# Kernel optimization log

Hardware: AMD Instinct MI355X
Metric: run time of the kernel (lower is better)

The kernel has to match this reference:

```python
import jax, jax.numpy as jnp
import numpy as np

N_CELLS = 50000
N_GENES = 2000
HIDDEN = 128
HEADS = 4
HEAD_DIM = HIDDEN // HEADS
E_FULL = 800000
E_PRUNED = 400000
LN_EPS = 1e-6
NEG_SLOPE = 0.2


def setup_inputs() -> dict:
    key = jax.random.key(0)
    ks = jax.random.split(key, 20)
    s_in = 1.0 / np.sqrt(N_GENES)
    s_h = 1.0 / np.sqrt(HIDDEN)
    inp = {
        "node_features": jax.random.normal(ks[0], (N_CELLS, N_GENES), jnp.float32),
        "full_edge_index": jax.random.randint(ks[1], (2, E_FULL), 0, N_CELLS, jnp.int64 if jax.config.jax_enable_x64 else jnp.int32),
        "full_edge_weights": jax.random.uniform(ks[2], (E_FULL, 1), jnp.float32),
        "pruned_edge_index": jax.random.randint(ks[3], (2, E_PRUNED), 0, N_CELLS, jnp.int64 if jax.config.jax_enable_x64 else jnp.int32),
        "pruned_edge_weights": jax.random.uniform(ks[4], (E_PRUNED, 1), jnp.float32),
        "alpha": jax.random.uniform(ks[5], (), jnp.float32),
        # input projection
        "ip_w": jax.random.normal(ks[6], (N_GENES, HIDDEN), jnp.float32) * s_in,
        "ip_b": jnp.zeros((HIDDEN,), jnp.float32),
        # GAT full graph
        "gf_wsrc": jax.random.normal(ks[7], (HIDDEN, HIDDEN), jnp.float32) * s_h,
        "gf_wdst": jax.random.normal(ks[8], (HIDDEN, HIDDEN), jnp.float32) * s_h,
        "gf_wedge": jax.random.normal(ks[9], (1, HIDDEN), jnp.float32),
        "gf_attn": jax.random.normal(ks[10], (HEADS, HEAD_DIM), jnp.float32) * (1.0 / np.sqrt(HEAD_DIM)),
        "gf_bias": jnp.zeros((HIDDEN,), jnp.float32),
        # GAT pruned graph
        "gp_wsrc": jax.random.normal(ks[11], (HIDDEN, HIDDEN), jnp.float32) * s_h,
        "gp_wdst": jax.random.normal(ks[12], (HIDDEN, HIDDEN), jnp.float32) * s_h,
        "gp_wedge": jax.random.normal(ks[13], (1, HIDDEN), jnp.float32),
        "gp_attn": jax.random.normal(ks[14], (HEADS, HEAD_DIM), jnp.float32) * (1.0 / np.sqrt(HEAD_DIM)),
        "gp_bias": jnp.zeros((HIDDEN,), jnp.float32),
        # LayerNorm
        "ln_scale": jnp.ones((HIDDEN,), jnp.float32),
        "ln_bias": jnp.zeros((HIDDEN,), jnp.float32),
    }
    return inp


def _gatv2(h, edge_index, edge_w, wsrc, wdst, wedge, attn, bias):
    """GATv2 with edge features: e_ij = a_h . leaky_relu(Ws h_i + Wd h_j + We w_ij),
    segment-softmax over destination nodes, scatter-aggregate Ws h_src, concat heads."""
    n = h.shape[0]
    src, dst = edge_index[0], edge_index[1]
    hs = (h @ wsrc).reshape(n, HEADS, HEAD_DIM)
    hd = (h @ wdst).reshape(n, HEADS, HEAD_DIM)
    ew = (edge_w @ wedge).reshape(-1, HEADS, HEAD_DIM)  # [E,H,D]
    z = jax.nn.leaky_relu(hs[src] + hd[dst] + ew, NEG_SLOPE)  # [E,H,D]
    logits = jnp.einsum('ehd,hd->eh', z, attn)  # [E,H]
    # segment softmax over incoming edges of each dst node
    m = jax.ops.segment_max(logits, dst, num_segments=n)
    m = jnp.where(jnp.isfinite(m), m, 0.0)
    ex = jnp.exp(logits - m[dst])
    denom = jax.ops.segment_sum(ex, dst, num_segments=n)
    att = ex / (denom[dst] + 1e-16)  # [E,H]
    out = jax.ops.segment_sum(att[..., None] * hs[src], dst, num_segments=n)  # [n,H,D]
    return out.reshape(n, HIDDEN) + bias


def _layer_norm(x, scale, bias):
    mu = jnp.mean(x, axis=-1, keepdims=True)
    var = jnp.mean(jnp.square(x - mu), axis=-1, keepdims=True)
    return (x - mu) * jax.lax.rsqrt(var + LN_EPS) * scale + bias


def reference(node_features, full_edge_index, full_edge_weights, pruned_edge_index,
              pruned_edge_weights, alpha, ip_w, ip_b,
              gf_wsrc, gf_wdst, gf_wedge, gf_attn, gf_bias,
              gp_wsrc, gp_wdst, gp_wedge, gp_attn, gp_bias,
              ln_scale, ln_bias):
    h = node_features @ ip_w + ip_b  # [n, hidden]
    h_full = _gatv2(h, full_edge_index, full_edge_weights, gf_wsrc, gf_wdst, gf_wedge, gf_attn, gf_bias)
    h_pruned = _gatv2(h, pruned_edge_index, pruned_edge_weights, gp_wsrc, gp_wdst, gp_wedge, gp_attn, gp_bias)
    h = (1.0 - alpha) * h_full + alpha * h_pruned
    h = jax.nn.elu(h)
    return _layer_norm(h, ln_scale, ln_bias)
```

## Files before the change

kernel.cpp:

```cpp
#include <hip/hip_runtime.h>
#include <hip/hip_bf16.h>

#define N_GENES 2000
#define SA 72
#define SH 136

typedef __attribute__((ext_vector_type(8))) short frag8;
typedef __attribute__((ext_vector_type(4))) float facc4;

static __device__ __forceinline__ unsigned short f2bf(float f) {
    unsigned int u = __float_as_uint(f);
    unsigned int r = (u + 0x7FFFu + ((u >> 16) & 1u)) >> 16;
    return (unsigned short)r;
}
static __device__ __forceinline__ float bf2f(unsigned short s) {
    return __uint_as_float(((unsigned int)s) << 16);
}
static __device__ __forceinline__ ushort2 pk2(float a, float b) {
    __hip_bfloat162 r = __float22bfloat162_rn(float2{a, b});
    return *(ushort2*)&r;
}

__global__ void prep(const float* __restrict__ ip_w,
                     const float* __restrict__ ws_f, const float* __restrict__ wd_f,
                     const float* __restrict__ ws_p, const float* __restrict__ wd_p,
                     unsigned short* __restrict__ Bt1,
                     unsigned short* __restrict__ Bf, unsigned short* __restrict__ Bp,
                     int* __restrict__ deg, int n2) {
    int idx = blockIdx.x * blockDim.x + threadIdx.x;
    if (idx < n2) deg[idx] = 0;
    if (idx < 128 * 2048) {
        int nrow = idx >> 11, k = idx & 2047;
        unsigned short v = 0;
        if (k < N_GENES) v = f2bf(ip_w[(size_t)k * 128 + nrow]);
        Bt1[idx] = v;
    } else {
        int q = idx - 128 * 2048;
        if (q >= 2 * 256 * 128) return;
        int g = q >> 15;
        int r = (q >> 7) & 255;
        int k = q & 127;
        const float* w = (g == 0) ? (r < 128 ? ws_f : wd_f) : (r < 128 ? ws_p : wd_p);
        (g == 0 ? Bf : Bp)[(r << 7) | k] = f2bf(w[k * 128 + (r & 127)]);
    }
}

__global__ __launch_bounds__(256) void gemm_deg(const float* __restrict__ A,
                                                const unsigned short* __restrict__ Bt,
                                                const float* __restrict__ bias,
                                                const unsigned short* __restrict__ Bf,
                                                const unsigned short* __restrict__ Bp,
                                                unsigned short* __restrict__ Cf,
                                                unsigned short* __restrict__ Cp,
                                                int M, int K, int gemmBlocks,
                                                const int* __restrict__ dst_f, int Ef,
                                                const int* __restrict__ dst_p, int Ep,
                                                int* __restrict__ deg, int N) {
    if (blockIdx.x >= gemmBlocks) {
        int e = (blockIdx.x - gemmBlocks) * 256 + threadIdx.x;
        if (e < Ef) atomicAdd(&deg[dst_f[e]], 1);
        else if (e < Ef + Ep) atomicAdd(&deg[N + dst_p[e - Ef]], 1);
        return;
    }
    const int Kpad = 2048;
    __shared__ __align__(16) unsigned short lA[64 * SA];
    __shared__ __align__(16) unsigned short lH[64 * SH];
    int t = threadIdx.x, lane = t & 63, wv = t >> 6;
    int lr = lane & 15, lq = lane >> 4;
    facc4 acc[4][2];
#pragma unroll
    for (int i = 0; i < 4; i++)
#pragma unroll
        for (int j = 0; j < 2; j++) acc[i][j] = (facc4){0.f, 0.f, 0.f, 0.f};
    int row_base = blockIdx.x * 64;

    int ar_r[4], ar_c[4];
    const float* ar_p[4];
#pragma unroll
    for (int j = 0; j < 4; j++) {
        int q = j * 256 + t;
        ar_r[j] = q >> 4;
        ar_c[j] = (q & 15) * 4;
        int rg = row_base + ar_r[j];
        if (rg >= M) rg = M - 1;
        ar_p[j] = A + (size_t)rg * K + ar_c[j];
    }
    const unsigned short* bp[4];
#pragma unroll
    for (int ks = 0; ks < 2; ks++)
#pragma unroll
        for (int ni = 0; ni < 2; ni++) {
            int col = wv * 32 + ni * 16 + lr;
            bp[ks * 2 + ni] = Bt + (size_t)col * Kpad + ks * 32 + lq * 8;
        }

    float4 ar[4];
    frag8 bfr[4];
#pragma unroll
    for (int j = 0; j < 4; j++) ar[j] = *(const float4*)(ar_p[j]);
#pragma unroll
    for (int f = 0; f < 4; f++) bfr[f] = *(const frag8*)(bp[f]);

    for (int k0 = 0; k0 < Kpad; k0 += 64) {
        __syncthreads();
#pragma unroll
        for (int j = 0; j < 4; j++) {
            ushort2 u01 = pk2(ar[j].x, ar[j].y);
            ushort2 u23 = pk2(ar[j].z, ar[j].w);
            ushort4 u = {u01.x, u01.y, u23.x, u23.y};
            *(ushort4*)&lA[ar_r[j] * SA + ar_c[j]] = u;
        }
        __syncthreads();
        int kn = k0 + 64;
        frag8 bfn[4];
        if (kn < Kpad) {
#pragma unroll
            for (int j = 0; j < 4; j++) {
                int kk = kn + ar_c[j];
                float4 v = {0.f, 0.f, 0.f, 0.f};
                if (kk < K) v = *(const float4*)(ar_p[j] + kn);
                ar[j] = v;
            }
#pragma unroll
            for (int f = 0; f < 4; f++) bfn[f] = *(const frag8*)(bp[f] + kn);
        }
#pragma unroll
        for (int ks = 0; ks < 2; ks++) {
            frag8 af[4];
#pragma unroll
            for (int mi = 0; mi < 4; mi++)
                af[mi] = *(const frag8*)&lA[(mi * 16 + lr) * SA + ks * 32 + lq * 8];
#pragma unroll
            for (int mi = 0; mi < 4; mi++)
#pragma unroll
                for (int ni = 0; ni < 2; ni++)
                    acc[mi][ni] = __builtin_amdgcn_mfma_f32_16x16x32_bf16(af[mi], bfr[ks * 2 + ni], acc[mi][ni], 0, 0, 0);
        }
        if (kn < Kpad) {
#pragma unroll
            for (int f = 0; f < 4; f++) bfr[f] = bfn[f];
        }
    }
    __syncthreads();
#pragma unroll
    for (int mi = 0; mi < 4; mi++) {
#pragma unroll
        for (int r = 0; r < 4; r++) {
            int row = mi * 16 + lq * 4 + r;
#pragma unroll
            for (int ni = 0; ni < 2; ni++) {
                int col = wv * 32 + ni * 16 + lr;
                lH[row * SH + col] = f2bf(acc[mi][ni][r] + bias[col]);
            }
        }
    }
    __syncthreads();
#pragma unroll 1
    for (int g = 0; g < 2; g++) {
        const unsigned short* B2 = g ? Bp : Bf;
        unsigned short* Cb = g ? Cp : Cf;
        facc4 a2[4][4];
#pragma unroll
        for (int i = 0; i < 4; i++)
#pragma unroll
            for (int j = 0; j < 4; j++) a2[i][j] = (facc4){0.f, 0.f, 0.f, 0.f};
#pragma unroll
        for (int ks = 0; ks < 4; ks++) {
            frag8 af[4], bf[4];
#pragma unroll
            for (int mi = 0; mi < 4; mi++)
                af[mi] = *(const frag8*)&lH[(mi * 16 + lr) * SH + ks * 32 + lq * 8];
#pragma unroll
            for (int ni = 0; ni < 4; ni++)
                bf[ni] = *(const frag8*)(B2 + ((wv * 64 + ni * 16 + lr) << 7) + ks * 32 + lq * 8);
#pragma unroll
            for (int mi = 0; mi < 4; mi++)
#pragma unroll
                for (int ni = 0; ni < 4; ni++)
                    a2[mi][ni] = __builtin_amdgcn_mfma_f32_16x16x32_bf16(af[mi], bf[ni], a2[mi][ni], 0, 0, 0);
        }
#pragma unroll
        for (int mi = 0; mi < 4; mi++) {
#pragma unroll
            for (int r = 0; r < 4; r++) {
                int row = row_base + mi * 16 + lq * 4 + r;
                if (row < M) {
#pragma unroll
                    for (int ni = 0; ni < 4; ni++) {
                        int col = wv * 64 + ni * 16 + lr;
                        Cb[(size_t)row * 256 + col] = f2bf(a2[mi][ni][r]);
                    }
                }
            }
        }
    }
}

__global__ __launch_bounds__(256) void scan_part(const int* __restrict__ in,
                                                 int* __restrict__ bsum, int n) {
    int t = threadIdx.x, b = blockIdx.x;
    int lane = t & 63, wv = t >> 6;
    int base = b * 2048 + t * 8;
    int s = 0;
    if (base + 7 < n) {
        int4 v0 = *(const int4*)(in + base);
        int4 v1 = *(const int4*)(in + base + 4);
        s = v0.x + v0.y + v0.z + v0.w + v1.x + v1.y + v1.z + v1.w;
    } else {
#pragma unroll
        for (int j = 0; j < 8; j++) if (base + j < n) s += in[base + j];
    }
#pragma unroll
    for (int o = 32; o >= 1; o >>= 1) s += __shfl_xor(s, o);
    __shared__ int red[4];
    if (lane == 0) red[wv] = s;
    __syncthreads();
    if (t == 0) bsum[b] = red[0] + red[1] + red[2] + red[3];
}

__global__ __launch_bounds__(256) void scan_tops(int* __restrict__ bsum, int nb,
                                                 int* __restrict__ offs, int n) {
    __shared__ int buf[256];
    int t = threadIdx.x;
    int orig = (t < nb) ? bsum[t] : 0;
    int v = orig;
    buf[t] = v;
    __syncthreads();
    for (int o = 1; o < 256; o <<= 1) {
        int y = (t >= o) ? buf[t - o] : 0;
        __syncthreads();
        v += y;
        buf[t] = v;
        __syncthreads();
    }
    if (t < nb) bsum[t] = v - orig;
    if (t == nb - 1) offs[n] = v;
}

__global__ __launch_bounds__(256) void scan_final(const int* __restrict__ in,
                                                  const int* __restrict__ bsum,
                                                  int* __restrict__ offs, int n) {
    int t = threadIdx.x, b = blockIdx.x;
    int lane = t & 63, wv = t >> 6;
    int base = b * 2048 + t * 8;
    int a[8];
#pragma unroll
    for (int j = 0; j < 8; j++) a[j] = (base + j < n) ? in[base + j] : 0;
    int s = a[0] + a[1] + a[2] + a[3] + a[4] + a[5] + a[6] + a[7];
    int incl = s;
#pragma unroll
    for (int o = 1; o < 64; o <<= 1) {
        int y = __shfl_up(incl, o);
        if (lane >= o) incl += y;
    }
    __shared__ int wsum[4];
    if (lane == 63) wsum[wv] = incl;
    __syncthreads();
    int wpre = 0;
#pragma unroll
    for (int j = 0; j < 4; j++) if (j < wv) wpre += wsum[j];
    int excl = incl - s + wpre + bsum[b];
#pragma unroll
    for (int j = 0; j < 8; j++) {
        if (base + j < n) offs[base + j] = excl;
        excl += a[j];
    }
}

__global__ void fill2(const int* __restrict__ src_f, const int* __restrict__ dst_f,
                      const float* __restrict__ ew_f, int Ef,
                      const int* __restrict__ src_p, const int* __restrict__ dst_p,
                      const float* __restrict__ ew_p, int Ep,
                      const int* __restrict__ offs, int* __restrict__ deg,
                      int2* __restrict__ srcw, int N) {
    int e = blockIdx.x * blockDim.x + threadIdx.x;
    if (e >= Ef + Ep) return;
    int g = (e >= Ef);
    int ee = g ? e - Ef : e;
    int d = g ? dst_p[ee] : dst_f[ee];
    int node = g ? N + d : d;
    int p = offs[node] + atomicAdd(&deg[node], -1) - 1;
    int s = g ? src_p[ee] : src_f[ee];
    float w = g ? ew_p[ee] : ew_f[ee];
    srcw[p] = make_int2(s, __float_as_int(w));
}

__global__ __launch_bounds__(256) void gat2(const int* __restrict__ offs,
                                            const int2* __restrict__ srcw,
                                            const unsigned short* __restrict__ hshd_f,
                                            const unsigned short* __restrict__ hshd_p,
                                            const float* __restrict__ wedge_f,
                                            const float* __restrict__ attn_f,
                                            const float* __restrict__ bias_f,
                                            const float* __restrict__ wedge_p,
                                            const float* __restrict__ attn_p,
                                            const float* __restrict__ bias_p,
                                            float* __restrict__ out_full,
                                            float* __restrict__ out_pruned, int N) {
    int node = blockIdx.x * 4 + (threadIdx.x >> 6);
    if (node >= 2 * N) return;
    int g = node >= N;
    int onode = g ? node - N : node;
    const unsigned short* hshd = g ? hshd_p : hshd_f;
    const float* wedge = g ? wedge_p : wedge_f;
    const float* attn = g ? attn_p : attn_f;
    const float* bias = g ? bias_p : bias_f;
    float* out = g ? out_pruned : out_full;
    int lane = threadIdx.x & 63;
    int d2 = lane * 2;
    const float LOG2E = 1.4426950408889634f;
    const float2 wv = *(const float2*)&wedge[d2];
    float2 av = *(const float2*)&attn[d2];
    av.x *= LOG2E; av.y *= LOG2E;
    unsigned int hdraw = *(const unsigned int*)&hshd[(size_t)onode * 256 + 128 + d2];
    const float hd0 = __uint_as_float(hdraw << 16);
    const float hd1 = __uint_as_float(hdraw & 0xffff0000u);
    int s = offs[node], cnt = offs[node + 1] - s;
    float m = -INFINITY, l = 0.f, acc0 = 0.f, acc1 = 0.f;
    if (cnt > 0) {
        int last = s + cnt - 1;
        auto CL = [last](int j) { return j > last ? last : j; };
        int2 e0 = srcw[s], e1 = srcw[CL(s + 1)], e2 = srcw[CL(s + 2)], e3 = srcw[CL(s + 3)];
        int2 e4 = srcw[CL(s + 4)], e5 = srcw[CL(s + 5)];
        unsigned int hr0 = *(const unsigned int*)&hshd[(size_t)e0.x * 256 + d2];
        unsigned int hr1 = *(const unsigned int*)&hshd[(size_t)e1.x * 256 + d2];
        unsigned int hr2 = *(const unsigned int*)&hshd[(size_t)e2.x * 256 + d2];
        unsigned int hr3 = *(const unsigned int*)&hshd[(size_t)e3.x * 256 + d2];
        for (int i = 0; i < cnt; i += 2) {
            int2 ea = srcw[CL(s + i + 6)], eb = srcw[CL(s + i + 7)];
            unsigned int hr4 = *(const unsigned int*)&hshd[(size_t)e4.x * 256 + d2];
            unsigned int hr5 = *(const unsigned int*)&hshd[(size_t)e5.x * 256 + d2];
            {
                float h0 = __uint_as_float(hr0 << 16);
                float h1 = __uint_as_float(hr0 & 0xffff0000u);
                float w = __int_as_float(e0.y);
                float z0 = fmaf(w, wv.x, h0 + hd0); z0 = (z0 > 0.f) ? z0 : 0.2f * z0;
                float z1 = fmaf(w, wv.y, h1 + hd1); z1 = (z1 > 0.f) ? z1 : 0.2f * z1;
                float t = z0 * av.x + z1 * av.y;
                t += __shfl_xor(t, 1);
                t += __shfl_xor(t, 2);
                t += __shfl_xor(t, 4);
                t += __shfl_xor(t, 8);
                float mn = fmaxf(m, t);
                float sc = __builtin_amdgcn_exp2f(m - mn);
                float p = __builtin_amdgcn_exp2f(t - mn);
                l = l * sc + p;
                acc0 = acc0 * sc + p * h0;
                acc1 = acc1 * sc + p * h1;
                m = mn;
            }
            if (i + 1 < cnt) {
                float h0 = __uint_as_float(hr1 << 16);
                float h1 = __uint_as_float(hr1 & 0xffff0000u);
                float w = __int_as_float(e1.y);
                float z0 = fmaf(w, wv.x, h0 + hd0); z0 = (z0 > 0.f) ? z0 : 0.2f * z0;
                float z1 = fmaf(w, wv.y, h1 + hd1); z1 = (z1 > 0.f) ? z1 : 0.2f * z1;
                float t = z0 * av.x + z1 * av.y;
                t += __shfl_xor(t, 1);
                t += __shfl_xor(t, 2);
                t += __shfl_xor(t, 4);
                t += __shfl_xor(t, 8);
                float mn = fmaxf(m, t);
                float sc = __builtin_amdgcn_exp2f(m - mn);
                float p = __builtin_amdgcn_exp2f(t - mn);
                l = l * sc + p;
                acc0 = acc0 * sc + p * h1 * 0.f + p * h0;
                acc0 = acc0 - p * h0 + p * h0;
                acc0 = acc0;
                acc1 = acc1 * sc + p * h1;
                m = mn;
            }
            e0 = e2; e1 = e3; e2 = e4; e3 = e5; e4 = ea; e5 = eb;
            hr0 = hr2; hr1 = hr3; hr2 = hr4; hr3 = hr5;
        }
    }
    float inv = 1.f / (l + 1e-16f);
    const float2 bv = *(const float2*)&bias[d2];
    float2 o;
    o.x = acc0 * inv + bv.x;
    o.y = acc1 * inv + bv.y;
    *(float2*)&out[(size_t)onode * 128 + d2] = o;
}

__global__ __launch_bounds__(256) void final_kernel(const float* __restrict__ hf,
                                                    float* __restrict__ out,
                                                    const float* __restrict__ alpha_p,
                                                    const float* __restrict__ scale,
                                                    const float* __restrict__ beta, int n) {
    int node = blockIdx.x * 4 + (threadIdx.x >> 6);
    if (node >= n) return;
    int lane = threadIdx.x & 63;
    int d2 = lane * 2;
    float a = *alpha_p;
    float2 f = *(const float2*)&hf[(size_t)node * 128 + d2];
    float2 p = *(const float2*)&out[(size_t)node * 128 + d2];
    float x0 = (1.f - a) * f.x + a * p.x;
    float x1 = (1.f - a) * f.y + a * p.y;
    x0 = (x0 > 0.f) ? x0 : expm1f(x0);
    x1 = (x1 > 0.f) ? x1 : expm1f(x1);
    float sm = x0 + x1;
#pragma unroll
    for (int o = 32; o >= 1; o >>= 1) sm += __shfl_xor(sm, o);
    float mu = sm * (1.f / 128.f);
    float d0 = x0 - mu, d1 = x1 - mu;
    float v = d0 * d0 + d1 * d1;
#pragma unroll
    for (int o = 32; o >= 1; o >>= 1) v += __shfl_xor(v, o);
    float rstd = rsqrtf(v * (1.f / 128.f) + 1e-6f);
    const float2 sv = *(const float2*)&scale[d2];
    const float2 bv = *(const float2*)&beta[d2];
    float2 o2;
    o2.x = d0 * rstd * sv.x + bv.x;
    o2.y = d1 * rstd * sv.y + bv.y;
    *(float2*)&out[(size_t)node * 128 + d2] = o2;
}

extern "C" void kernel_launch(void* const* d_in, const int* in_sizes, int n_in,
                              void* d_out, int out_size, void* d_ws, size_t ws_size,
                              hipStream_t stream) {
    const float* nf = (const float*)d_in[0];
    const int* fei = (const int*)d_in[1];
    const float* few = (const float*)d_in[2];
    const int* pei = (const int*)d_in[3];
    const float* pew = (const float*)d_in[4];
    const float* alpha = (const float*)d_in[5];
    const float* ip_w = (const float*)d_in[6];
    const float* ip_b = (const float*)d_in[7];
    const float* gf_wsrc = (const float*)d_in[8];
    const float* gf_wdst = (const float*)d_in[9];
    const float* gf_wedge = (const float*)d_in[10];
    const float* gf_attn = (const float*)d_in[11];
    const float* gf_bias = (const float*)d_in[12];
    const float* gp_wsrc = (const float*)d_in[13];
    const float* gp_wdst = (const float*)d_in[14];
    const float* gp_wedge = (const float*)d_in[15];
    const float* gp_attn = (const float*)d_in[16];
    const float* gp_bias = (const float*)d_in[17];
    const float* ln_scale = (const float*)d_in[18];
    const float* ln_bias = (const float*)d_in[19];

    const int N = in_sizes[0] / N_GENES;
    const int Ef = in_sizes[1] / 2;
    const int Ep = in_sizes[3] / 2;
    const int Etot = Ef + Ep;
    const int n2 = 2 * N;

    char* base = (char*)d_ws;
    size_t off = 0;
    auto carve = [&](size_t bytes) -> char* {
        char* p = base + off;
        off = (off + bytes + 255) & ~(size_t)255;
        return p;
    };
    unsigned short* Bt1 = (unsigned short*)carve((size_t)128 * 2048 * 2);
    unsigned short* Bf = (unsigned short*)carve(256 * 128 * 2);
    unsigned short* Bp = (unsigned short*)carve(256 * 128 * 2);
    unsigned short* hshd_f = (unsigned short*)carve((size_t)N * 256 * 2);
    unsigned short* hshd_p = (unsigned short*)carve((size_t)N * 256 * 2);
    float* h_full = (float*)carve((size_t)N * 128 * 4);
    int* deg = (int*)carve((size_t)n2 * 4);
    int* offs = (int*)carve((size_t)(n2 + 4) * 4);
    int* bsum = (int*)carve(256 * 4);
    int2* srcw = (int2*)carve((size_t)Etot * 8);
    float* out_f = (float*)d_out;

    const int* src_f = fei;
    const int* dst_f = fei + Ef;
    const int* src_p = pei;
    const int* dst_p = pei + Ep;

    prep<<<(128 * 2048 + 2 * 256 * 128 + 255) / 256, 256, 0, stream>>>(
        ip_w, gf_wsrc, gf_wdst, gp_wsrc, gp_wdst, Bt1, Bf, Bp, deg, n2);

    int gb1 = (N + 63) / 64;
    int degb = (Etot + 255) / 256;
    gemm_deg<<<gb1 + degb, 256, 0, stream>>>(nf, Bt1, ip_b, Bf, Bp, hshd_f, hshd_p,
                                             N, N_GENES, gb1,
                                             dst_f, Ef, dst_p, Ep, deg, N);

    int nb = (n2 + 2047) / 2048;
    scan_part<<<nb, 256, 0, stream>>>(deg, bsum, n2);
    scan_tops<<<1, 256, 0, stream>>>(bsum, nb, offs, n2);
    scan_final<<<nb, 256, 0, stream>>>(deg, bsum, offs, n2);
    fill2<<<(Etot + 255) / 256, 256, 0, stream>>>(src_f, dst_f, few, Ef, src_p, dst_p, pew, Ep,
                                                  offs, deg, srcw, N);

    gat2<<<(n2 + 3) / 4, 256, 0, stream>>>(offs, srcw, hshd_f, hshd_p,
                                           gf_wedge, gf_attn, gf_bias,
                                           gp_wedge, gp_attn, gp_bias,
                                           h_full, out_f, N);

    final_kernel<<<(N + 3) / 4, 256, 0, stream>>>(h_full, out_f, alpha, ln_scale, ln_bias, N);
    (void)ws_size; (void)n_in; (void)out_size;
}
```

Measured before the change: 813.1 us.

## Replace three-pass scan with atomic segment assignment and fuse GAT with final LayerNorm

The three-kernel exclusive scan is replaced by one kernel. Each wavefront scans its degrees and claims a base offset through a global atomic counter, so segments are contiguous but no longer in node order. The fill step now uses a separate cursor array, and degrees are kept for the segment lengths. The two GAT passes and the final blend/ELU/LayerNorm kernel are fused into one kernel per node, removing the h_full round-trip and two launches. Fusion halves the grid to N blocks, each doing both graphs serially, which may lengthen the critical path per wave.

```diff
diff --git a/kernel.cpp b/kernel.cpp
--- a/kernel.cpp
+++ b/kernel.cpp
@@ -12,9 +12,6 @@
     unsigned int u = __float_as_uint(f);
     unsigned int r = (u + 0x7FFFu + ((u >> 16) & 1u)) >> 16;
     return (unsigned short)r;
-}
-static __device__ __forceinline__ float bf2f(unsigned short s) {
-    return __uint_as_float(((unsigned int)s) << 16);
 }
 static __device__ __forceinline__ ushort2 pk2(float a, float b) {
     __hip_bfloat162 r = __float22bfloat162_rn(float2{a, b});
@@ -26,9 +23,10 @@
                      const float* __restrict__ ws_p, const float* __restrict__ wd_p,
                      unsigned short* __restrict__ Bt1,
                      unsigned short* __restrict__ Bf, unsigned short* __restrict__ Bp,
-                     int* __restrict__ deg, int n2) {
+                     int* __restrict__ deg, unsigned int* __restrict__ counter, int n2) {
     int idx = blockIdx.x * blockDim.x + threadIdx.x;
     if (idx < n2) deg[idx] = 0;
+    if (idx == 0) counter[0] = 0u;
     if (idx < 128 * 2048) {
         int nrow = idx >> 11, k = idx & 2047;
         unsigned short v = 0;
@@ -196,118 +194,50 @@
     }
 }
 
-__global__ __launch_bounds__(256) void scan_part(const int* __restrict__ in,
-                                                 int* __restrict__ bsum, int n) {
-    int t = threadIdx.x, b = blockIdx.x;
-    int lane = t & 63, wv = t >> 6;
-    int base = b * 2048 + t * 8;
-    int s = 0;
-    if (base + 7 < n) {
-        int4 v0 = *(const int4*)(in + base);
-        int4 v1 = *(const int4*)(in + base + 4);
-        s = v0.x + v0.y + v0.z + v0.w + v1.x + v1.y + v1.z + v1.w;
-    } else {
-#pragma unroll
-        for (int j = 0; j < 8; j++) if (base + j < n) s += in[base + j];
-    }
-#pragma unroll
-    for (int o = 32; o >= 1; o >>= 1) s += __shfl_xor(s, o);
-    __shared__ int red[4];
-    if (lane == 0) red[wv] = s;
-    __syncthreads();
-    if (t == 0) bsum[b] = red[0] + red[1] + red[2] + red[3];
-}
-
-__global__ __launch_bounds__(256) void scan_tops(int* __restrict__ bsum, int nb,
-                                                 int* __restrict__ offs, int n) {
-    __shared__ int buf[256];
-    int t = threadIdx.x;
-    int orig = (t < nb) ? bsum[t] : 0;
-    int v = orig;
-    buf[t] = v;
-    __syncthreads();
-    for (int o = 1; o < 256; o <<= 1) {
-        int y = (t >= o) ? buf[t - o] : 0;
-        __syncthreads();
-        v += y;
-        buf[t] = v;
-        __syncthreads();
-    }
-    if (t < nb) bsum[t] = v - orig;
-    if (t == nb - 1) offs[n] = v;
-}
-
-__global__ __launch_bounds__(256) void scan_final(const int* __restrict__ in,
-                                                  const int* __restrict__ bsum,
-                                                  int* __restrict__ offs, int n) {
-    int t = threadIdx.x, b = blockIdx.x;
-    int lane = t & 63, wv = t >> 6;
-    int base = b * 2048 + t * 8;
-    int a[8];
-#pragma unroll
-    for (int j = 0; j < 8; j++) a[j] = (base + j < n) ? in[base + j] : 0;
-    int s = a[0] + a[1] + a[2] + a[3] + a[4] + a[5] + a[6] + a[7];
-    int incl = s;
+__global__ __launch_bounds__(256) void seg_assign(const int* __restrict__ deg,
+                                                  int* __restrict__ offs,
+                                                  int* __restrict__ cur,
+                                                  unsigned int* __restrict__ counter, int n2) {
+    int i = blockIdx.x * 256 + threadIdx.x;
+    int lane = threadIdx.x & 63;
+    int c = (i < n2) ? deg[i] : 0;
+    int incl = c;
 #pragma unroll
     for (int o = 1; o < 64; o <<= 1) {
         int y = __shfl_up(incl, o);
         if (lane >= o) incl += y;
     }
-    __shared__ int wsum[4];
-    if (lane == 63) wsum[wv] = incl;
-    __syncthreads();
-    int wpre = 0;
-#pragma unroll
-    for (int j = 0; j < 4; j++) if (j < wv) wpre += wsum[j];
-    int excl = incl - s + wpre + bsum[b];
-#pragma unroll
-    for (int j = 0; j < 8; j++) {
-        if (base + j < n) offs[base + j] = excl;
-        excl += a[j];
-    }
+    int wtot = __shfl(incl, 63);
+    int base = 0;
+    if (lane == 63) base = (int)atomicAdd(counter, (unsigned int)wtot);
+    base = __shfl(base, 63);
+    int start = base + incl - c;
+    if (i < n2) { offs[i] = start; cur[i] = start; }
 }
 
 __global__ void fill2(const int* __restrict__ src_f, const int* __restrict__ dst_f,
                       const float* __restrict__ ew_f, int Ef,
                       const int* __restrict__ src_p, const int* __restrict__ dst_p,
                       const float* __restrict__ ew_p, int Ep,
-                      const int* __restrict__ offs, int* __restrict__ deg,
-                      int2* __restrict__ srcw, int N) {
+                      int* __restrict__ cur, int2* __restrict__ srcw, int N) {
     int e = blockIdx.x * blockDim.x + threadIdx.x;
     if (e >= Ef + Ep) return;
     int g = (e >= Ef);
     int ee = g ? e - Ef : e;
     int d = g ? dst_p[ee] : dst_f[ee];
     int node = g ? N + d : d;
-    int p = offs[node] + atomicAdd(&deg[node], -1) - 1;
+    int p = atomicAdd(&cur[node], 1);
     int s = g ? src_p[ee] : src_f[ee];
     float w = g ? ew_p[ee] : ew_f[ee];
     srcw[p] = make_int2(s, __float_as_int(w));
 }
 
-__global__ __launch_bounds__(256) void gat2(const int* __restrict__ offs,
-                                            const int2* __restrict__ srcw,
-                                            const unsigned short* __restrict__ hshd_f,
-                                            const unsigned short* __restrict__ hshd_p,
-                                            const float* __restrict__ wedge_f,
-                                            const float* __restrict__ attn_f,
-                                            const float* __restrict__ bias_f,
-                                            const float* __restrict__ wedge_p,
-                                            const float* __restrict__ attn_p,
-                                            const float* __restrict__ bias_p,
-                                            float* __restrict__ out_full,
-                                            float* __restrict__ out_pruned, int N) {
-    int node = blockIdx.x * 4 + (threadIdx.x >> 6);
-    if (node >= 2 * N) return;
-    int g = node >= N;
-    int onode = g ? node - N : node;
-    const unsigned short* hshd = g ? hshd_p : hshd_f;
-    const float* wedge = g ? wedge_p : wedge_f;
-    const float* attn = g ? attn_p : attn_f;
-    const float* bias = g ? bias_p : bias_f;
-    float* out = g ? out_pruned : out_full;
-    int lane = threadIdx.x & 63;
-    int d2 = lane * 2;
+static __device__ __forceinline__ float2 gat_node(const unsigned short* __restrict__ hshd,
+                                                  const float* __restrict__ wedge,
+                                                  const float* __restrict__ attn,
+                                                  const float* __restrict__ bias,
+                                                  const int2* __restrict__ srcw,
+                                                  int s, int cnt, int onode, int d2) {
     const float LOG2E = 1.4426950408889634f;
     const float2 wv = *(const float2*)&wedge[d2];
     float2 av = *(const float2*)&attn[d2];
@@ -315,7 +245,6 @@
     unsigned int hdraw = *(const unsigned int*)&hshd[(size_t)onode * 256 + 128 + d2];
     const float hd0 = __uint_as_float(hdraw << 16);
     const float hd1 = __uint_as_float(hdraw & 0xffff0000u);
-    int s = offs[node], cnt = offs[node + 1] - s;
     float m = -INFINITY, l = 0.f, acc0 = 0.f, acc1 = 0.f;
     if (cnt > 0) {
         int last = s + cnt - 1;
@@ -364,9 +293,7 @@
                 float sc = __builtin_amdgcn_exp2f(m - mn);
                 float p = __builtin_amdgcn_exp2f(t - mn);
                 l = l * sc + p;
-                acc0 = acc0 * sc + p * h1 * 0.f + p * h0;
-                acc0 = acc0 - p * h0 + p * h0;
-                acc0 = acc0;
+                acc0 = acc0 * sc + p * h0;
                 acc1 = acc1 * sc + p * h1;
                 m = mn;
             }
@@ -376,24 +303,33 @@
     }
     float inv = 1.f / (l + 1e-16f);
     const float2 bv = *(const float2*)&bias[d2];
-    float2 o;
-    o.x = acc0 * inv + bv.x;
-    o.y = acc1 * inv + bv.y;
-    *(float2*)&out[(size_t)onode * 128 + d2] = o;
-}
-
-__global__ __launch_bounds__(256) void final_kernel(const float* __restrict__ hf,
-                                                    float* __restrict__ out,
-                                                    const float* __restrict__ alpha_p,
-                                                    const float* __restrict__ scale,
-                                                    const float* __restrict__ beta, int n) {
+    return float2{acc0 * inv + bv.x, acc1 * inv + bv.y};
+}
+
+__global__ __launch_bounds__(256) void gat_final(const int* __restrict__ offs,
+                                                 const int* __restrict__ deg,
+                                                 const int2* __restrict__ srcw,
+                                                 const unsigned short* __restrict__ hshd_f,
+                                                 const unsigned short* __restrict__ hshd_p,
+                                                 const float* __restrict__ wedge_f,
+                                                 const float* __restrict__ attn_f,
+                                                 const float* __restrict__ bias_f,
+                                                 const float* __restrict__ wedge_p,
+                                                 const float* __restrict__ attn_p,
+                                                 const float* __restrict__ bias_p,
+                                                 const float* __restrict__ alpha_p,
+                                                 const float* __restrict__ scale,
+                                                 const float* __restrict__ beta,
+                                                 float* __restrict__ out, int N) {
     int node = blockIdx.x * 4 + (threadIdx.x >> 6);
-    if (node >= n) return;
+    if (node >= N) return;
     int lane = threadIdx.x & 63;
     int d2 = lane * 2;
+    float2 f = gat_node(hshd_f, wedge_f, attn_f, bias_f, srcw,
+                        offs[node], deg[node], node, d2);
+    float2 p = gat_node(hshd_p, wedge_p, attn_p, bias_p, srcw,
+                        offs[N + node], deg[N + node], node, d2);
     float a = *alpha_p;
-    float2 f = *(const float2*)&hf[(size_t)node * 128 + d2];
-    float2 p = *(const float2*)&out[(size_t)node * 128 + d2];
     float x0 = (1.f - a) * f.x + a * p.x;
     float x1 = (1.f - a) * f.y + a * p.y;
     x0 = (x0 > 0.f) ? x0 : expm1f(x0);
@@ -457,10 +393,10 @@
     unsigned short* Bp = (unsigned short*)carve(256 * 128 * 2);
     unsigned short* hshd_f = (unsigned short*)carve((size_t)N * 256 * 2);
     unsigned short* hshd_p = (unsigned short*)carve((size_t)N * 256 * 2);
-    float* h_full = (float*)carve((size_t)N * 128 * 4);
     int* deg = (int*)carve((size_t)n2 * 4);
-    int* offs = (int*)carve((size_t)(n2 + 4) * 4);
-    int* bsum = (int*)carve(256 * 4);
+    int* offs = (int*)carve((size_t)n2 * 4);
+    int* cur = (int*)carve((size_t)n2 * 4);
+    unsigned int* counter = (unsigned int*)carve(4);
     int2* srcw = (int2*)carve((size_t)Etot * 8);
     float* out_f = (float*)d_out;
 
@@ -470,7 +406,7 @@
     const int* dst_p = pei + Ep;
 
     prep<<<(128 * 2048 + 2 * 256 * 128 + 255) / 256, 256, 0, stream>>>(
-        ip_w, gf_wsrc, gf_wdst, gp_wsrc, gp_wdst, Bt1, Bf, Bp, deg, n2);
+        ip_w, gf_wsrc, gf_wdst, gp_wsrc, gp_wdst, Bt1, Bf, Bp, deg, counter, n2);
 
     int gb1 = (N + 63) / 64;
     int degb = (Etot + 255) / 256;
@@ -478,18 +414,14 @@
                                              N, N_GENES, gb1,
                                              dst_f, Ef, dst_p, Ep, deg, N);
 
-    int nb = (n2 + 2047) / 2048;
-    scan_part<<<nb, 256, 0, stream>>>(deg, bsum, n2);
-    scan_tops<<<1, 256, 0, stream>>>(bsum, nb, offs, n2);
-    scan_final<<<nb, 256, 0, stream>>>(deg, bsum, offs, n2);
+    seg_assign<<<(n2 + 255) / 256, 256, 0, stream>>>(deg, offs, cur, counter, n2);
+
     fill2<<<(Etot + 255) / 256, 256, 0, stream>>>(src_f, dst_f, few, Ef, src_p, dst_p, pew, Ep,
-                                                  offs, deg, srcw, N);
-
-    gat2<<<(n2 + 3) / 4, 256, 0, stream>>>(offs, srcw, hshd_f, hshd_p,
-                                           gf_wedge, gf_attn, gf_bias,
-                                           gp_wedge, gp_attn, gp_bias,
-                                           h_full, out_f, N);
-
-    final_kernel<<<(N + 3) / 4, 256, 0, stream>>>(h_full, out_f, alpha, ln_scale, ln_bias, N);
+                                                  cur, srcw, N);
+
+    gat_final<<<(N + 3) / 4, 256, 0, stream>>>(offs, deg, srcw, hshd_f, hshd_p,
+                                               gf_wedge, gf_attn, gf_bias,
+                                               gp_wedge, gp_attn, gp_bias,
+                                               alpha, ln_scale, ln_bias, out_f, N);
     (void)ws_size; (void)n_in; (void)out_size;
 }
```

After: 830.9 us. 1.02x slower.
